# Kernel tuning notes

Measured on AMD Instinct MI355X. Metric: run time of the kernel, lower is better.

## Reference

```python
import jax, jax.numpy as jnp
import numpy as np

HEADS = 8
DIM = 64  # per-head dim; scale = (DIM / HEADS) ** 0.5 as in the original (unusual but faithful)


def setup_inputs() -> dict:
    key = jax.random.key(0)
    b, L = 4, 2048
    C = 3 * HEADS * DIM  # 1536, channels-first input
    x = jax.random.normal(key, (b, C, L), dtype=jnp.float32)
    return {"x": x}


def reference(x):
    b, C, L = x.shape
    scale = (DIM / HEADS) ** 0.5
    # [b, C, L] -> [b, L, 3, h, d] -> [b, 3, h, L, d]
    xt = jnp.swapaxes(x, -1, -2).reshape(b, L, 3, HEADS, DIM)
    xt = jnp.transpose(xt, (0, 2, 3, 1, 4))
    q, k, v = xt[:, 0], xt[:, 1], xt[:, 2]  # each [b, h, L, d]
    qk = jnp.einsum('bhid,bhjd->bhij', q, k) / scale  # [b, h, L, L]
    qk = jax.nn.softmax(qk, axis=-1)
    o = jnp.einsum('bhij,bhjd->bhid', qk, v)  # [b, h, L, d]
    o = jnp.transpose(o, (0, 2, 1, 3)).reshape(b, L, HEADS * DIM)
    return (jnp.swapaxes(o, -1, -2), qk)  # ([b, h*d, L], [b, h, L, L])
```

## Files before the change

### kernel.cpp

```cpp
#include <hip/hip_runtime.h>
#include <hip/hip_bf16.h>

#define BB 4
#define HH 8
#define LL 2048
#define DD 64

typedef __attribute__((ext_vector_type(8))) short short8;
typedef __attribute__((ext_vector_type(4))) float floatx4;
typedef unsigned int u32;
typedef unsigned short u16;
typedef unsigned long long u64;

#define SM_COEF 0.51006977f

#define WAITV(N) asm volatile("s_waitcnt vmcnt(" #N ")" ::: "memory")
#define LGKM0()  asm volatile("s_waitcnt lgkmcnt(0)" ::: "memory")
#define SCHED0() __builtin_amdgcn_sched_barrier(0)

__device__ __forceinline__ void gld_lds16(const void* g, void* l) {
  __builtin_amdgcn_global_load_lds((const __attribute__((address_space(1))) u32*)g,
                                   (__attribute__((address_space(3))) u32*)l, 16, 0, 0);
}

__global__ __launch_bounds__(256) void qk_tr_kernel(const float* __restrict__ x,
                                                    unsigned short* __restrict__ ws) {
  const int b = blockIdx.z;
  const int g = blockIdx.y >> 3;
  const int h = blockIdx.y & 7;
  const int tid = threadIdx.x;
  const int i = blockIdx.x * 64 + (tid & 63);
  const int dq = tid >> 6;
  const float scale = (g == 0) ? SM_COEF : 1.0f;
  const float* src = x + ((size_t)(b * 1536 + g * 512 + h * 64 + dq * 16)) * LL + i;
  float v[16];
#pragma unroll
  for (int k = 0; k < 16; ++k) v[k] = src[(size_t)k * LL];
  __hip_bfloat16 hb[16] __attribute__((aligned(16)));
#pragma unroll
  for (int k = 0; k < 16; ++k) hb[k] = __float2bfloat16(v[k] * scale);
  unsigned short* dst = ws + (size_t)g * ((size_t)BB * HH * LL * DD) +
                        ((size_t)(b * HH + h) * LL + i) * DD + dq * 16;
  *reinterpret_cast<short8*>(dst) = *reinterpret_cast<const short8*>(hb);
  *reinterpret_cast<short8*>(dst + 8) = *reinterpret_cast<const short8*>(hb + 8);
}

__global__ __launch_bounds__(256) void v_cv_kernel(const float* __restrict__ x,
                                                   unsigned short* __restrict__ vt) {
  const size_t idx = ((size_t)blockIdx.x * 256 + threadIdx.x) * 4;
  const size_t row = idx >> 11;
  const int col = (int)(idx & 2047);
  const size_t b = row >> 9;
  const size_t r = row & 511;
  const float4 f = *reinterpret_cast<const float4*>(x + ((b * 1536 + 1024 + r) << 11) + col);
  __hip_bfloat16 hb[4] __attribute__((aligned(8)));
  hb[0] = __float2bfloat16(f.x);
  hb[1] = __float2bfloat16(f.y);
  hb[2] = __float2bfloat16(f.z);
  hb[3] = __float2bfloat16(f.w);
  *reinterpret_cast<u64*>(vt + idx) = *reinterpret_cast<const u64*>(hb);
}

__global__ __launch_bounds__(256, 2) void sums_kernel(const u16* __restrict__ qb,
                                                      const u16* __restrict__ kb,
                                                      float* __restrict__ mneg) {
  __shared__ u16 kbuf[2][8192] __attribute__((aligned(16)));

  const int wg = blockIdx.x;
  const int lin = (wg & 7) * 64 + (wg >> 3);
  const int bh = lin >> 4;
  const int ib = lin & 15;

  const int tid = threadIdx.x;
  const int wave = tid >> 6, lane = tid & 63;
  const int l15 = lane & 15, g = lane >> 4;
  const int swz = (l15 & 7) << 4;
  const int itile = ib * 128 + wave * 32;

  const u16* qrA = qb + ((size_t)bh * LL + itile + l15) * DD + 8 * g;
  const u16* qrB = qrA + 16 * DD;
  const short8 qa0 = *reinterpret_cast<const short8*>(qrA);
  const short8 qa1 = *reinterpret_cast<const short8*>(qrA + 32);
  const short8 qb0 = *reinterpret_cast<const short8*>(qrB);
  const short8 qb1 = *reinterpret_cast<const short8*>(qrB + 32);
  const u16* ktile = kb + (size_t)bh * LL * DD;

  auto stageK = [&](int bsel, int tidx) {
    const char* src = (const char*)(ktile + (size_t)tidx * 128 * DD);
#pragma unroll
    for (int q = 0; q < 4; ++q) {
      const int o = wave * 4096 + q * 1024 + lane * 16;
      const int row = o >> 7;
      const int so = (o & ~127) | ((o & 127) ^ ((row & 7) << 4));
      gld_lds16(src + so, (char*)(&kbuf[bsel][0]) + wave * 4096 + q * 1024);
    }
  };

  float lsA0 = 0.f, lsA1 = 0.f, lsB0 = 0.f, lsB1 = 0.f;
  stageK(0, 0);
  for (int t = 0; t < 16; ++t) {
    WAITV(0);
    __builtin_amdgcn_s_barrier();
    SCHED0();
    stageK((t + 1) & 1, (t + 1) & 15);
    const char* kbb = (const char*)(&kbuf[t & 1][0]);
#pragma unroll
    for (int nt = 0; nt < 8; ++nt) {
      const char* kr = kbb + (nt * 16 + l15) * 128;
      const short8 kf0 = *reinterpret_cast<const short8*>(kr + ((g * 16) ^ swz));
      const short8 kf1 = *reinterpret_cast<const short8*>(kr + ((64 + g * 16) ^ swz));
      floatx4 accA = {0.f, 0.f, 0.f, 0.f}, accB = {0.f, 0.f, 0.f, 0.f};
      accA = __builtin_amdgcn_mfma_f32_16x16x32_bf16(kf0, qa0, accA, 0, 0, 0);
      accA = __builtin_amdgcn_mfma_f32_16x16x32_bf16(kf1, qa1, accA, 0, 0, 0);
      accB = __builtin_amdgcn_mfma_f32_16x16x32_bf16(kf0, qb0, accB, 0, 0, 0);
      accB = __builtin_amdgcn_mfma_f32_16x16x32_bf16(kf1, qb1, accB, 0, 0, 0);
      if (nt & 1) {
#pragma unroll
        for (int r = 0; r < 4; ++r) {
          lsA1 += __builtin_amdgcn_exp2f(accA[r]);
          lsB1 += __builtin_amdgcn_exp2f(accB[r]);
        }
      } else {
#pragma unroll
        for (int r = 0; r < 4; ++r) {
          lsA0 += __builtin_amdgcn_exp2f(accA[r]);
          lsB0 += __builtin_amdgcn_exp2f(accB[r]);
        }
      }
    }
  }
  float lsA = lsA0 + lsA1, lsB = lsB0 + lsB1;
  lsA += __shfl_xor(lsA, 16, 64);
  lsA += __shfl_xor(lsA, 32, 64);
  lsB += __shfl_xor(lsB, 16, 64);
  lsB += __shfl_xor(lsB, 32, 64);
  if (g == 0) {
    mneg[(size_t)bh * LL + itile + l15] = -__log2f(lsA);
    mneg[(size_t)bh * LL + itile + 16 + l15] = -__log2f(lsB);
  }
}

__global__ __launch_bounds__(256, 2) void mha_write_kernel(const u16* __restrict__ qb,
                                                           const u16* __restrict__ kb,
                                                           const u16* __restrict__ vt,
                                                           const float* __restrict__ mneg,
                                                           float* __restrict__ out) {
  __shared__ u16 kbuf[2][8192] __attribute__((aligned(16)));
  __shared__ unsigned char pls[4][4096] __attribute__((aligned(16)));

  const int wg = blockIdx.x;
  const int lin = (wg & 7) * 64 + (wg >> 3);
  const int bh = lin >> 4;
  const int ib = lin & 15;
  const int b = bh >> 3, h = bh & 7;

  const int tid = threadIdx.x;
  const int wave = tid >> 6, lane = tid & 63;
  const int l15 = lane & 15, g = lane >> 4;
  const int swz = (l15 & 7) << 4;
  const int itile = ib * 128 + wave * 32;

  const u16* qrA = qb + ((size_t)bh * LL + itile + l15) * DD + 8 * g;
  const u16* qrB = qrA + 16 * DD;
  const short8 qa0 = *reinterpret_cast<const short8*>(qrA);
  const short8 qa1 = *reinterpret_cast<const short8*>(qrA + 32);
  const short8 qb0 = *reinterpret_cast<const short8*>(qrB);
  const short8 qb1 = *reinterpret_cast<const short8*>(qrB + 32);
  const u16* ktile = kb + (size_t)bh * LL * DD;
  const u16* vbase = vt + (size_t)bh * DD * LL;
  const float mnA = mneg[(size_t)bh * LL + itile + l15];
  const float mnB = mneg[(size_t)bh * LL + itile + 16 + l15];

  auto stageK = [&](int bsel, int tidx) {
    const char* src = (const char*)(ktile + (size_t)tidx * 128 * DD);
#pragma unroll
    for (int q = 0; q < 4; ++q) {
      const int o = wave * 4096 + q * 1024 + lane * 16;
      const int row = o >> 7;
      const int so = (o & ~127) | ((o & 127) ^ ((row & 7) << 4));
      gld_lds16(src + so, (char*)(&kbuf[bsel][0]) + wave * 4096 + q * 1024);
    }
  };

  floatx4 oaccA[4], oaccB[4];
#pragma unroll
  for (int mt = 0; mt < 4; ++mt) {
    oaccA[mt] = (floatx4){0.f, 0.f, 0.f, 0.f};
    oaccB[mt] = (floatx4){0.f, 0.f, 0.f, 0.f};
  }

  const int srow = lane >> 4;
  const int scol = (lane & 15) * 4;
  float* pbase = out + (size_t)BB * 512 * LL + ((size_t)bh * LL + itile) * LL;
  unsigned char* wb = &pls[wave][0];

  stageK(0, 0);
  for (int t = 0; t < 16; ++t) {
    if (t == 0) { WAITV(0); } else { WAITV(16); }
    __builtin_amdgcn_s_barrier();
    SCHED0();
    const int j0 = t * 128;
    short8 vf0a[4], vf0b[4], vf1a[4], vf1b[4];
    {
      const u16* vc0 = vbase + (size_t)l15 * LL + j0 + 8 * g;
      const u16* vc1 = vc0 + 64;
#pragma unroll
      for (int mt = 0; mt < 4; ++mt) {
        vf0a[mt] = *reinterpret_cast<const short8*>(vc0 + (size_t)mt * 16 * LL);
        vf0b[mt] = *reinterpret_cast<const short8*>(vc0 + (size_t)mt * 16 * LL + 32);
      }
#pragma unroll
      for (int mt = 0; mt < 4; ++mt) {
        vf1a[mt] = *reinterpret_cast<const short8*>(vc1 + (size_t)mt * 16 * LL);
        vf1b[mt] = *reinterpret_cast<const short8*>(vc1 + (size_t)mt * 16 * LL + 32);
      }
    }
    SCHED0();
    stageK((t + 1) & 1, (t + 1) & 15);
    SCHED0();
    const char* kbb = (const char*)(&kbuf[t & 1][0]);

#pragma unroll
    for (int hf = 0; hf < 2; ++hf) {
      const int jh = j0 + hf * 64;
#pragma unroll
      for (int nt = 0; nt < 4; ++nt) {
        const char* kr = kbb + ((hf * 64 + nt * 16) + l15) * 128;
        const short8 kf0 = *reinterpret_cast<const short8*>(kr + ((g * 16) ^ swz));
        const short8 kf1 = *reinterpret_cast<const short8*>(kr + ((64 + g * 16) ^ swz));
        floatx4 accA = {0.f, 0.f, 0.f, 0.f}, accB = {0.f, 0.f, 0.f, 0.f};
        accA = __builtin_amdgcn_mfma_f32_16x16x32_bf16(kf0, qa0, accA, 0, 0, 0);
        accA = __builtin_amdgcn_mfma_f32_16x16x32_bf16(kf1, qa1, accA, 0, 0, 0);
        accB = __builtin_amdgcn_mfma_f32_16x16x32_bf16(kf0, qb0, accB, 0, 0, 0);
        accB = __builtin_amdgcn_mfma_f32_16x16x32_bf16(kf1, qb1, accB, 0, 0, 0);
        __hip_bfloat16 ha[4] __attribute__((aligned(8))), hbv[4] __attribute__((aligned(8)));
#pragma unroll
        for (int r = 0; r < 4; ++r) {
          ha[r]  = __float2bfloat16(__builtin_amdgcn_exp2f(accA[r] + mnA));
          hbv[r] = __float2bfloat16(__builtin_amdgcn_exp2f(accB[r] + mnB));
        }
        *reinterpret_cast<u64*>(wb + l15 * 128 + ((nt * 32 + g * 8) ^ swz)) =
            *reinterpret_cast<const u64*>(ha);
        *reinterpret_cast<u64*>(wb + (16 + l15) * 128 + ((nt * 32 + g * 8) ^ swz)) =
            *reinterpret_cast<const u64*>(hbv);
      }
      LGKM0();
      SCHED0();
#pragma unroll
      for (int k = 0; k < 8; ++k) {
        const int row = k * 4 + srow;
        const u64 pk = *reinterpret_cast<const u64*>(
            wb + row * 128 + ((scol * 2) ^ ((row & 7) << 4)));
        const u16* pp = (const u16*)&pk;
        float4 pw;
        pw.x = __uint_as_float((u32)pp[0] << 16);
        pw.y = __uint_as_float((u32)pp[1] << 16);
        pw.z = __uint_as_float((u32)pp[2] << 16);
        pw.w = __uint_as_float((u32)pp[3] << 16);
        *reinterpret_cast<float4*>(pbase + (size_t)row * LL + jh + scol) = pw;
      }
      WAITV(20);
      SCHED0();
#pragma unroll
      for (int ks = 0; ks < 2; ++ks) {
        const short8 pbA = *reinterpret_cast<const short8*>(
            wb + l15 * 128 + ((ks * 64 + g * 16) ^ swz));
        const short8 pbB = *reinterpret_cast<const short8*>(
            wb + (16 + l15) * 128 + ((ks * 64 + g * 16) ^ swz));
#pragma unroll
        for (int mt = 0; mt < 4; ++mt) {
          const short8 vv = hf == 0 ? (ks == 0 ? vf0a[mt] : vf0b[mt])
                                    : (ks == 0 ? vf1a[mt] : vf1b[mt]);
          oaccA[mt] = __builtin_amdgcn_mfma_f32_16x16x32_bf16(vv, pbA, oaccA[mt], 0, 0, 0);
          oaccB[mt] = __builtin_amdgcn_mfma_f32_16x16x32_bf16(vv, pbB, oaccB[mt], 0, 0, 0);
        }
      }
    }
  }

  float* obA = out + (size_t)(b * 512 + h * 64) * LL + itile + l15;
  float* obB = obA + 16;
#pragma unroll
  for (int mt = 0; mt < 4; ++mt) {
#pragma unroll
    for (int r = 0; r < 4; ++r) {
      obA[(size_t)(mt * 16 + 4 * g + r) * LL] = oaccA[mt][r];
      obB[(size_t)(mt * 16 + 4 * g + r) * LL] = oaccB[mt][r];
    }
  }
}

extern "C" void kernel_launch(void* const* d_in, const int* in_sizes, int n_in,
                              void* d_out, int out_size, void* d_ws, size_t ws_size,
                              hipStream_t stream) {
  const float* x = (const float*)d_in[0];
  float* out = (float*)d_out;
  unsigned short* ws = (unsigned short*)d_ws;
  unsigned short* qbuf = ws;
  unsigned short* kbuf = ws + (size_t)BB * HH * LL * DD;
  unsigned short* vbuf = ws + (size_t)2 * BB * HH * LL * DD;
  float* mneg = (float*)(ws + (size_t)3 * BB * HH * LL * DD);

  qk_tr_kernel<<<dim3(32, 16, 4), 256, 0, stream>>>(x, ws);
  v_cv_kernel<<<dim3(4096), 256, 0, stream>>>(x, vbuf);
  sums_kernel<<<dim3(512), 256, 0, stream>>>(qbuf, kbuf, mneg);
  mha_write_kernel<<<dim3(512), 256, 0, stream>>>(qbuf, kbuf, vbuf, mneg, out);
}
```

Baseline: 191.0 us.

## Split key range across two workgroups with atomic output accumulation and triple-buffered K

The main attention-write kernel now splits each query tile's key range in half across two workgroups, doubling the grid to 1024 blocks. The partial P·V outputs are combined with float atomic adds into an output that is zeroed by a memset. The K staging tile is halved and triple-buffered, and occupancy is raised to 4 blocks per SM. The sums kernel also switches to a triple-buffered K pipeline. This is meant to fix poor occupancy and load balance with only 512 blocks, at the cost of atomics, an extra memset, and nondeterministic summation order.

```diff
diff --git a/kernel.cpp b/kernel.cpp
--- a/kernel.cpp
+++ b/kernel.cpp
@@ -64,7 +64,7 @@
 __global__ __launch_bounds__(256, 2) void sums_kernel(const u16* __restrict__ qb,
                                                       const u16* __restrict__ kb,
                                                       float* __restrict__ mneg) {
-  __shared__ u16 kbuf[2][8192] __attribute__((aligned(16)));
+  __shared__ u16 kbuf[3][8192] __attribute__((aligned(16)));
 
   const int wg = blockIdx.x;
   const int lin = (wg & 7) * 64 + (wg >> 3);
@@ -98,12 +98,13 @@
 
   float lsA0 = 0.f, lsA1 = 0.f, lsB0 = 0.f, lsB1 = 0.f;
   stageK(0, 0);
+  stageK(1, 1);
   for (int t = 0; t < 16; ++t) {
-    WAITV(0);
+    WAITV(4);
     __builtin_amdgcn_s_barrier();
     SCHED0();
-    stageK((t + 1) & 1, (t + 1) & 15);
-    const char* kbb = (const char*)(&kbuf[t & 1][0]);
+    stageK((t + 2) % 3, (t + 2) & 15);
+    const char* kbb = (const char*)(&kbuf[t % 3][0]);
 #pragma unroll
     for (int nt = 0; nt < 8; ++nt) {
       const char* kr = kbb + (nt * 16 + l15) * 128;
@@ -140,18 +141,20 @@
   }
 }
 
-__global__ __launch_bounds__(256, 2) void mha_write_kernel(const u16* __restrict__ qb,
+__global__ __launch_bounds__(256, 4) void mha_write_kernel(const u16* __restrict__ qb,
                                                            const u16* __restrict__ kb,
                                                            const u16* __restrict__ vt,
                                                            const float* __restrict__ mneg,
                                                            float* __restrict__ out) {
-  __shared__ u16 kbuf[2][8192] __attribute__((aligned(16)));
+  __shared__ u16 kbuf[3][4096] __attribute__((aligned(16)));
   __shared__ unsigned char pls[4][4096] __attribute__((aligned(16)));
 
   const int wg = blockIdx.x;
-  const int lin = (wg & 7) * 64 + (wg >> 3);
-  const int bh = lin >> 4;
-  const int ib = lin & 15;
+  const int lin = (wg & 7) * 128 + (wg >> 3);
+  const int bh = lin >> 5;
+  const int ib = (lin >> 1) & 15;
+  const int jsel = lin & 1;
+  const int jbase = jsel * 1024;
   const int b = bh >> 3, h = bh & 7;
 
   const int tid = threadIdx.x;
@@ -166,19 +169,19 @@
   const short8 qa1 = *reinterpret_cast<const short8*>(qrA + 32);
   const short8 qb0 = *reinterpret_cast<const short8*>(qrB);
   const short8 qb1 = *reinterpret_cast<const short8*>(qrB + 32);
-  const u16* ktile = kb + (size_t)bh * LL * DD;
-  const u16* vbase = vt + (size_t)bh * DD * LL;
+  const u16* ktile = kb + (size_t)bh * LL * DD + (size_t)jbase * DD;
+  const u16* vbase = vt + (size_t)bh * DD * LL + jbase;
   const float mnA = mneg[(size_t)bh * LL + itile + l15];
   const float mnB = mneg[(size_t)bh * LL + itile + 16 + l15];
 
   auto stageK = [&](int bsel, int tidx) {
-    const char* src = (const char*)(ktile + (size_t)tidx * 128 * DD);
-#pragma unroll
-    for (int q = 0; q < 4; ++q) {
-      const int o = wave * 4096 + q * 1024 + lane * 16;
+    const char* src = (const char*)(ktile + (size_t)tidx * 64 * DD);
+#pragma unroll
+    for (int q = 0; q < 2; ++q) {
+      const int o = wave * 2048 + q * 1024 + lane * 16;
       const int row = o >> 7;
       const int so = (o & ~127) | ((o & 127) ^ ((row & 7) << 4));
-      gld_lds16(src + so, (char*)(&kbuf[bsel][0]) + wave * 4096 + q * 1024);
+      gld_lds16(src + so, (char*)(&kbuf[bsel][0]) + wave * 2048 + q * 1024);
     }
   };
 
@@ -191,89 +194,79 @@
 
   const int srow = lane >> 4;
   const int scol = (lane & 15) * 4;
-  float* pbase = out + (size_t)BB * 512 * LL + ((size_t)bh * LL + itile) * LL;
+  float* pbase = out + (size_t)BB * 512 * LL + ((size_t)bh * LL + itile) * LL + jbase;
   unsigned char* wb = &pls[wave][0];
 
   stageK(0, 0);
+  stageK(1, 1);
   for (int t = 0; t < 16; ++t) {
-    if (t == 0) { WAITV(0); } else { WAITV(16); }
+    if (t == 0) { WAITV(2); }
     __builtin_amdgcn_s_barrier();
     SCHED0();
-    const int j0 = t * 128;
-    short8 vf0a[4], vf0b[4], vf1a[4], vf1b[4];
+    const int j0 = t * 64;
+    short8 vfa[4], vfb[4];
     {
-      const u16* vc0 = vbase + (size_t)l15 * LL + j0 + 8 * g;
-      const u16* vc1 = vc0 + 64;
+      const u16* vc = vbase + (size_t)l15 * LL + j0 + 8 * g;
 #pragma unroll
       for (int mt = 0; mt < 4; ++mt) {
-        vf0a[mt] = *reinterpret_cast<const short8*>(vc0 + (size_t)mt * 16 * LL);
-        vf0b[mt] = *reinterpret_cast<const short8*>(vc0 + (size_t)mt * 16 * LL + 32);
+        vfa[mt] = *reinterpret_cast<const short8*>(vc + (size_t)mt * 16 * LL);
+        vfb[mt] = *reinterpret_cast<const short8*>(vc + (size_t)mt * 16 * LL + 32);
       }
+    }
+    SCHED0();
+    stageK((t + 2) % 3, (t + 2) & 15);
+    SCHED0();
+    const char* kbb = (const char*)(&kbuf[t % 3][0]);
+
+#pragma unroll
+    for (int nt = 0; nt < 4; ++nt) {
+      const char* kr = kbb + (nt * 16 + l15) * 128;
+      const short8 kf0 = *reinterpret_cast<const short8*>(kr + ((g * 16) ^ swz));
+      const short8 kf1 = *reinterpret_cast<const short8*>(kr + ((64 + g * 16) ^ swz));
+      floatx4 accA = {0.f, 0.f, 0.f, 0.f}, accB = {0.f, 0.f, 0.f, 0.f};
+      accA = __builtin_amdgcn_mfma_f32_16x16x32_bf16(kf0, qa0, accA, 0, 0, 0);
+      accA = __builtin_amdgcn_mfma_f32_16x16x32_bf16(kf1, qa1, accA, 0, 0, 0);
+      accB = __builtin_amdgcn_mfma_f32_16x16x32_bf16(kf0, qb0, accB, 0, 0, 0);
+      accB = __builtin_amdgcn_mfma_f32_16x16x32_bf16(kf1, qb1, accB, 0, 0, 0);
+      __hip_bfloat16 ha[4] __attribute__((aligned(8))), hbv[4] __attribute__((aligned(8)));
+#pragma unroll
+      for (int r = 0; r < 4; ++r) {
+        ha[r]  = __float2bfloat16(__builtin_amdgcn_exp2f(accA[r] + mnA));
+        hbv[r] = __float2bfloat16(__builtin_amdgcn_exp2f(accB[r] + mnB));
+      }
+      *reinterpret_cast<u64*>(wb + l15 * 128 + ((nt * 32 + g * 8) ^ swz)) =
+          *reinterpret_cast<const u64*>(ha);
+      *reinterpret_cast<u64*>(wb + (16 + l15) * 128 + ((nt * 32 + g * 8) ^ swz)) =
+          *reinterpret_cast<const u64*>(hbv);
+    }
+    LGKM0();
+    SCHED0();
+#pragma unroll
+    for (int k = 0; k < 8; ++k) {
+      const int row = k * 4 + srow;
+      const u64 pk = *reinterpret_cast<const u64*>(
+          wb + row * 128 + ((scol * 2) ^ ((row & 7) << 4)));
+      const u16* pp = (const u16*)&pk;
+      float4 pw;
+      pw.x = __uint_as_float((u32)pp[0] << 16);
+      pw.y = __uint_as_float((u32)pp[1] << 16);
+      pw.z = __uint_as_float((u32)pp[2] << 16);
+      pw.w = __uint_as_float((u32)pp[3] << 16);
+      *reinterpret_cast<float4*>(pbase + (size_t)row * LL + j0 + scol) = pw;
+    }
+    WAITV(10);
+    SCHED0();
+#pragma unroll
+    for (int ks = 0; ks < 2; ++ks) {
+      const short8 pbA = *reinterpret_cast<const short8*>(
+          wb + l15 * 128 + ((ks * 64 + g * 16) ^ swz));
+      const short8 pbB = *reinterpret_cast<const short8*>(
+          wb + (16 + l15) * 128 + ((ks * 64 + g * 16) ^ swz));
 #pragma unroll
       for (int mt = 0; mt < 4; ++mt) {
-        vf1a[mt] = *reinterpret_cast<const short8*>(vc1 + (size_t)mt * 16 * LL);
-        vf1b[mt] = *reinterpret_cast<const short8*>(vc1 + (size_t)mt * 16 * LL + 32);
-      }
-    }
-    SCHED0();
-    stageK((t + 1) & 1, (t + 1) & 15);
-    SCHED0();
-    const char* kbb = (const char*)(&kbuf[t & 1][0]);
-
-#pragma unroll
-    for (int hf = 0; hf < 2; ++hf) {
-      const int jh = j0 + hf * 64;
-#pragma unroll
-      for (int nt = 0; nt < 4; ++nt) {
-        const char* kr = kbb + ((hf * 64 + nt * 16) + l15) * 128;
-        const short8 kf0 = *reinterpret_cast<const short8*>(kr + ((g * 16) ^ swz));
-        const short8 kf1 = *reinterpret_cast<const short8*>(kr + ((64 + g * 16) ^ swz));
-        floatx4 accA = {0.f, 0.f, 0.f, 0.f}, accB = {0.f, 0.f, 0.f, 0.f};
-        accA = __builtin_amdgcn_mfma_f32_16x16x32_bf16(kf0, qa0, accA, 0, 0, 0);
-        accA = __builtin_amdgcn_mfma_f32_16x16x32_bf16(kf1, qa1, accA, 0, 0, 0);
-        accB = __builtin_amdgcn_mfma_f32_16x16x32_bf16(kf0, qb0, accB, 0, 0, 0);
-        accB = __builtin_amdgcn_mfma_f32_16x16x32_bf16(kf1, qb1, accB, 0, 0, 0);
-        __hip_bfloat16 ha[4] __attribute__((aligned(8))), hbv[4] __attribute__((aligned(8)));
-#pragma unroll
-        for (int r = 0; r < 4; ++r) {
-          ha[r]  = __float2bfloat16(__builtin_amdgcn_exp2f(accA[r] + mnA));
-          hbv[r] = __float2bfloat16(__builtin_amdgcn_exp2f(accB[r] + mnB));
-        }
-        *reinterpret_cast<u64*>(wb + l15 * 128 + ((nt * 32 + g * 8) ^ swz)) =
-            *reinterpret_cast<const u64*>(ha);
-        *reinterpret_cast<u64*>(wb + (16 + l15) * 128 + ((nt * 32 + g * 8) ^ swz)) =
-            *reinterpret_cast<const u64*>(hbv);
-      }
-      LGKM0();
-      SCHED0();
-#pragma unroll
-      for (int k = 0; k < 8; ++k) {
-        const int row = k * 4 + srow;
-        const u64 pk = *reinterpret_cast<const u64*>(
-            wb + row * 128 + ((scol * 2) ^ ((row & 7) << 4)));
-        const u16* pp = (const u16*)&pk;
-        float4 pw;
-        pw.x = __uint_as_float((u32)pp[0] << 16);
-        pw.y = __uint_as_float((u32)pp[1] << 16);
-        pw.z = __uint_as_float((u32)pp[2] << 16);
-        pw.w = __uint_as_float((u32)pp[3] << 16);
-        *reinterpret_cast<float4*>(pbase + (size_t)row * LL + jh + scol) = pw;
-      }
-      WAITV(20);
-      SCHED0();
-#pragma unroll
-      for (int ks = 0; ks < 2; ++ks) {
-        const short8 pbA = *reinterpret_cast<const short8*>(
-            wb + l15 * 128 + ((ks * 64 + g * 16) ^ swz));
-        const short8 pbB = *reinterpret_cast<const short8*>(
-            wb + (16 + l15) * 128 + ((ks * 64 + g * 16) ^ swz));
-#pragma unroll
-        for (int mt = 0; mt < 4; ++mt) {
-          const short8 vv = hf == 0 ? (ks == 0 ? vf0a[mt] : vf0b[mt])
-                                    : (ks == 0 ? vf1a[mt] : vf1b[mt]);
-          oaccA[mt] = __builtin_amdgcn_mfma_f32_16x16x32_bf16(vv, pbA, oaccA[mt], 0, 0, 0);
-          oaccB[mt] = __builtin_amdgcn_mfma_f32_16x16x32_bf16(vv, pbB, oaccB[mt], 0, 0, 0);
-        }
+        const short8 vv = ks == 0 ? vfa[mt] : vfb[mt];
+        oaccA[mt] = __builtin_amdgcn_mfma_f32_16x16x32_bf16(vv, pbA, oaccA[mt], 0, 0, 0);
+        oaccB[mt] = __builtin_amdgcn_mfma_f32_16x16x32_bf16(vv, pbB, oaccB[mt], 0, 0, 0);
       }
     }
   }
@@ -284,8 +277,8 @@
   for (int mt = 0; mt < 4; ++mt) {
 #pragma unroll
     for (int r = 0; r < 4; ++r) {
-      obA[(size_t)(mt * 16 + 4 * g + r) * LL] = oaccA[mt][r];
-      obB[(size_t)(mt * 16 + 4 * g + r) * LL] = oaccB[mt][r];
+      unsafeAtomicAdd(&obA[(size_t)(mt * 16 + 4 * g + r) * LL], oaccA[mt][r]);
+      unsafeAtomicAdd(&obB[(size_t)(mt * 16 + 4 * g + r) * LL], oaccB[mt][r]);
     }
   }
 }
@@ -301,8 +294,9 @@
   unsigned short* vbuf = ws + (size_t)2 * BB * HH * LL * DD;
   float* mneg = (float*)(ws + (size_t)3 * BB * HH * LL * DD);
 
+  hipMemsetAsync(out, 0, (size_t)BB * 512 * LL * sizeof(float), stream);
   qk_tr_kernel<<<dim3(32, 16, 4), 256, 0, stream>>>(x, ws);
   v_cv_kernel<<<dim3(4096), 256, 0, stream>>>(x, vbuf);
   sums_kernel<<<dim3(512), 256, 0, stream>>>(qbuf, kbuf, mneg);
-  mha_write_kernel<<<dim3(512), 256, 0, stream>>>(qbuf, kbuf, vbuf, mneg, out);
-}
+  mha_write_kernel<<<dim3(1024), 256, 0, stream>>>(qbuf, kbuf, vbuf, mneg, out);
+}
```

Result: slower. 216.0 us (+13.1%).

## Stage V tiles through LDS with triple-buffered 64-key K/V pipeline

Applied to the files above, without the earlier changes.

V fragments were loaded straight from global memory into registers on every tile; now both K and V are staged into LDS with async global-to-LDS loads. The loop uses 64-key tiles and a three-deep buffer, prefetching two tiles ahead. The aim is to hide the latency of the V loads and free the registers that held V. In exchange the loop has twice as many iterations and barriers, plus extra LDS traffic and a larger LDS footprint that could limit occupancy.

```diff
diff --git a/kernel.cpp b/kernel.cpp
--- a/kernel.cpp
+++ b/kernel.cpp
@@ -145,7 +145,8 @@
                                                            const u16* __restrict__ vt,
                                                            const float* __restrict__ mneg,
                                                            float* __restrict__ out) {
-  __shared__ u16 kbuf[2][8192] __attribute__((aligned(16)));
+  __shared__ u16 kbuf[3][4096] __attribute__((aligned(16)));
+  __shared__ u16 vlds[3][4096] __attribute__((aligned(16)));
   __shared__ unsigned char pls[4][4096] __attribute__((aligned(16)));
 
   const int wg = blockIdx.x;
@@ -172,13 +173,24 @@
   const float mnB = mneg[(size_t)bh * LL + itile + 16 + l15];
 
   auto stageK = [&](int bsel, int tidx) {
-    const char* src = (const char*)(ktile + (size_t)tidx * 128 * DD);
-#pragma unroll
-    for (int q = 0; q < 4; ++q) {
-      const int o = wave * 4096 + q * 1024 + lane * 16;
+    const char* src = (const char*)(ktile + (size_t)tidx * 64 * DD);
+#pragma unroll
+    for (int q = 0; q < 2; ++q) {
+      const int o = wave * 2048 + q * 1024 + lane * 16;
       const int row = o >> 7;
       const int so = (o & ~127) | ((o & 127) ^ ((row & 7) << 4));
-      gld_lds16(src + so, (char*)(&kbuf[bsel][0]) + wave * 4096 + q * 1024);
+      gld_lds16(src + so, (char*)(&kbuf[bsel][0]) + wave * 2048 + q * 1024);
+    }
+  };
+  auto stageV = [&](int bsel, int tidx) {
+    const char* src = (const char*)vbase + (size_t)tidx * 128;
+#pragma unroll
+    for (int q = 0; q < 2; ++q) {
+      const int o = wave * 2048 + q * 1024 + lane * 16;
+      const int row = o >> 7;
+      const int scol = (o & 127) ^ ((row & 7) << 4);
+      gld_lds16(src + (size_t)row * (LL * 2) + scol,
+                (char*)(&vlds[bsel][0]) + wave * 2048 + q * 1024);
     }
   };
 
@@ -194,86 +206,68 @@
   float* pbase = out + (size_t)BB * 512 * LL + ((size_t)bh * LL + itile) * LL;
   unsigned char* wb = &pls[wave][0];
 
-  stageK(0, 0);
-  for (int t = 0; t < 16; ++t) {
-    if (t == 0) { WAITV(0); } else { WAITV(16); }
+  stageK(0, 0); stageV(0, 0);
+  stageK(1, 1); stageV(1, 1);
+  for (int t = 0; t < 32; ++t) {
+    if (t == 0) { WAITV(4); } else if (t == 1) { WAITV(12); } else { WAITV(20); }
     __builtin_amdgcn_s_barrier();
     SCHED0();
-    const int j0 = t * 128;
-    short8 vf0a[4], vf0b[4], vf1a[4], vf1b[4];
-    {
-      const u16* vc0 = vbase + (size_t)l15 * LL + j0 + 8 * g;
-      const u16* vc1 = vc0 + 64;
+    stageK((t + 2) % 3, (t + 2) & 31);
+    stageV((t + 2) % 3, (t + 2) & 31);
+    SCHED0();
+    const int j0 = t * 64;
+    const char* kbb = (const char*)(&kbuf[t % 3][0]);
+    const char* vbb = (const char*)(&vlds[t % 3][0]);
+
+#pragma unroll
+    for (int nt = 0; nt < 4; ++nt) {
+      const char* kr = kbb + (nt * 16 + l15) * 128;
+      const short8 kf0 = *reinterpret_cast<const short8*>(kr + ((g * 16) ^ swz));
+      const short8 kf1 = *reinterpret_cast<const short8*>(kr + ((64 + g * 16) ^ swz));
+      floatx4 accA = {0.f, 0.f, 0.f, 0.f}, accB = {0.f, 0.f, 0.f, 0.f};
+      accA = __builtin_amdgcn_mfma_f32_16x16x32_bf16(kf0, qa0, accA, 0, 0, 0);
+      accA = __builtin_amdgcn_mfma_f32_16x16x32_bf16(kf1, qa1, accA, 0, 0, 0);
+      accB = __builtin_amdgcn_mfma_f32_16x16x32_bf16(kf0, qb0, accB, 0, 0, 0);
+      accB = __builtin_amdgcn_mfma_f32_16x16x32_bf16(kf1, qb1, accB, 0, 0, 0);
+      __hip_bfloat16 ha[4] __attribute__((aligned(8))), hbv[4] __attribute__((aligned(8)));
+#pragma unroll
+      for (int r = 0; r < 4; ++r) {
+        ha[r]  = __float2bfloat16(__builtin_amdgcn_exp2f(accA[r] + mnA));
+        hbv[r] = __float2bfloat16(__builtin_amdgcn_exp2f(accB[r] + mnB));
+      }
+      *reinterpret_cast<u64*>(wb + l15 * 128 + ((nt * 32 + g * 8) ^ swz)) =
+          *reinterpret_cast<const u64*>(ha);
+      *reinterpret_cast<u64*>(wb + (16 + l15) * 128 + ((nt * 32 + g * 8) ^ swz)) =
+          *reinterpret_cast<const u64*>(hbv);
+    }
+    LGKM0();
+    SCHED0();
+#pragma unroll
+    for (int k = 0; k < 8; ++k) {
+      const int row = k * 4 + srow;
+      const u64 pk = *reinterpret_cast<const u64*>(
+          wb + row * 128 + ((scol * 2) ^ ((row & 7) << 4)));
+      const u16* pp = (const u16*)&pk;
+      float4 pw;
+      pw.x = __uint_as_float((u32)pp[0] << 16);
+      pw.y = __uint_as_float((u32)pp[1] << 16);
+      pw.z = __uint_as_float((u32)pp[2] << 16);
+      pw.w = __uint_as_float((u32)pp[3] << 16);
+      *reinterpret_cast<float4*>(pbase + (size_t)row * LL + j0 + scol) = pw;
+    }
+#pragma unroll
+    for (int ks = 0; ks < 2; ++ks) {
+      const short8 pbA = *reinterpret_cast<const short8*>(
+          wb + l15 * 128 + ((ks * 64 + g * 16) ^ swz));
+      const short8 pbB = *reinterpret_cast<const short8*>(
+          wb + (16 + l15) * 128 + ((ks * 64 + g * 16) ^ swz));
 #pragma unroll
       for (int mt = 0; mt < 4; ++mt) {
-        vf0a[mt] = *reinterpret_cast<const short8*>(vc0 + (size_t)mt * 16 * LL);
-        vf0b[mt] = *reinterpret_cast<const short8*>(vc0 + (size_t)mt * 16 * LL + 32);
-      }
-#pragma unroll
-      for (int mt = 0; mt < 4; ++mt) {
-        vf1a[mt] = *reinterpret_cast<const short8*>(vc1 + (size_t)mt * 16 * LL);
-        vf1b[mt] = *reinterpret_cast<const short8*>(vc1 + (size_t)mt * 16 * LL + 32);
-      }
-    }
-    SCHED0();
-    stageK((t + 1) & 1, (t + 1) & 15);
-    SCHED0();
-    const char* kbb = (const char*)(&kbuf[t & 1][0]);
-
-#pragma unroll
-    for (int hf = 0; hf < 2; ++hf) {
-      const int jh = j0 + hf * 64;
-#pragma unroll
-      for (int nt = 0; nt < 4; ++nt) {
-        const char* kr = kbb + ((hf * 64 + nt * 16) + l15) * 128;
-        const short8 kf0 = *reinterpret_cast<const short8*>(kr + ((g * 16) ^ swz));
-        const short8 kf1 = *reinterpret_cast<const short8*>(kr + ((64 + g * 16) ^ swz));
-        floatx4 accA = {0.f, 0.f, 0.f, 0.f}, accB = {0.f, 0.f, 0.f, 0.f};
-        accA = __builtin_amdgcn_mfma_f32_16x16x32_bf16(kf0, qa0, accA, 0, 0, 0);
-        accA = __builtin_amdgcn_mfma_f32_16x16x32_bf16(kf1, qa1, accA, 0, 0, 0);
-        accB = __builtin_amdgcn_mfma_f32_16x16x32_bf16(kf0, qb0, accB, 0, 0, 0);
-        accB = __builtin_amdgcn_mfma_f32_16x16x32_bf16(kf1, qb1, accB, 0, 0, 0);
-        __hip_bfloat16 ha[4] __attribute__((aligned(8))), hbv[4] __attribute__((aligned(8)));
-#pragma unroll
-        for (int r = 0; r < 4; ++r) {
-          ha[r]  = __float2bfloat16(__builtin_amdgcn_exp2f(accA[r] + mnA));
-          hbv[r] = __float2bfloat16(__builtin_amdgcn_exp2f(accB[r] + mnB));
-        }
-        *reinterpret_cast<u64*>(wb + l15 * 128 + ((nt * 32 + g * 8) ^ swz)) =
-            *reinterpret_cast<const u64*>(ha);
-        *reinterpret_cast<u64*>(wb + (16 + l15) * 128 + ((nt * 32 + g * 8) ^ swz)) =
-            *reinterpret_cast<const u64*>(hbv);
-      }
-      LGKM0();
-      SCHED0();
-#pragma unroll
-      for (int k = 0; k < 8; ++k) {
-        const int row = k * 4 + srow;
-        const u64 pk = *reinterpret_cast<const u64*>(
-            wb + row * 128 + ((scol * 2) ^ ((row & 7) << 4)));
-        const u16* pp = (const u16*)&pk;
-        float4 pw;
-        pw.x = __uint_as_float((u32)pp[0] << 16);
-        pw.y = __uint_as_float((u32)pp[1] << 16);
-        pw.z = __uint_as_float((u32)pp[2] << 16);
-        pw.w = __uint_as_float((u32)pp[3] << 16);
-        *reinterpret_cast<float4*>(pbase + (size_t)row * LL + jh + scol) = pw;
-      }
-      WAITV(20);
-      SCHED0();
-#pragma unroll
-      for (int ks = 0; ks < 2; ++ks) {
-        const short8 pbA = *reinterpret_cast<const short8*>(
-            wb + l15 * 128 + ((ks * 64 + g * 16) ^ swz));
-        const short8 pbB = *reinterpret_cast<const short8*>(
-            wb + (16 + l15) * 128 + ((ks * 64 + g * 16) ^ swz));
-#pragma unroll
-        for (int mt = 0; mt < 4; ++mt) {
-          const short8 vv = hf == 0 ? (ks == 0 ? vf0a[mt] : vf0b[mt])
-                                    : (ks == 0 ? vf1a[mt] : vf1b[mt]);
-          oaccA[mt] = __builtin_amdgcn_mfma_f32_16x16x32_bf16(vv, pbA, oaccA[mt], 0, 0, 0);
-          oaccB[mt] = __builtin_amdgcn_mfma_f32_16x16x32_bf16(vv, pbB, oaccB[mt], 0, 0, 0);
-        }
+        const int vrow = mt * 16 + l15;
+        const short8 vv = *reinterpret_cast<const short8*>(
+            vbb + vrow * 128 + ((ks * 64 + g * 16) ^ ((vrow & 7) << 4)));
+        oaccA[mt] = __builtin_amdgcn_mfma_f32_16x16x32_bf16(vv, pbA, oaccA[mt], 0, 0, 0);
+        oaccB[mt] = __builtin_amdgcn_mfma_f32_16x16x32_bf16(vv, pbB, oaccB[mt], 0, 0, 0);
       }
     }
   }
```

Result: slower. 198.1 us (+3.7%).
